# Kernel optimization log

Hardware: AMD Instinct MI355X
Metric: run time of the kernel (lower is better)

## Reference

```python
import jax, jax.numpy as jnp
import numpy as np

UNITS = 128

def setup_inputs() -> dict:
    key = jax.random.key(0)
    ks = jax.random.split(key, 8)
    B, Te, Td, De, Dd = 4, 512, 256, 512, 512
    enc = jax.random.normal(ks[0], (B, Te, De), dtype=jnp.float32)
    dec = jax.random.normal(ks[1], (B, Td, Dd), dtype=jnp.float32)
    # Dense params (glorot-ish scale)
    W1_w = jax.random.normal(ks[2], (De, UNITS), dtype=jnp.float32) / np.sqrt(De)
    W1_b = jnp.zeros((UNITS,), dtype=jnp.float32)
    W2_w = jax.random.normal(ks[3], (Dd, UNITS), dtype=jnp.float32) / np.sqrt(Dd)
    W2_b = jnp.zeros((UNITS,), dtype=jnp.float32)
    V_w = jax.random.normal(ks[4], (UNITS, 1), dtype=jnp.float32) / np.sqrt(UNITS)
    V_b = jnp.zeros((1,), dtype=jnp.float32)
    return {"encoder_out": enc, "decoder_out": dec,
            "W1_w": W1_w, "W1_b": W1_b, "W2_w": W2_w, "W2_b": W2_b,
            "V_w": V_w, "V_b": V_b}

def reference(encoder_out, decoder_out, W1_w, W1_b, W2_w, W2_b, V_w, V_b):
    # Project once per side (faithful: Dense is applied to broadcasted tensors,
    # but Dense commutes with broadcasting so projecting first is identical math).
    enc_p = jnp.einsum('bed,du->beu', encoder_out, W1_w) + W1_b   # [B,Te,U]
    dec_p = jnp.einsum('btd,du->btu', decoder_out, W2_w) + W2_b   # [B,Td,U]
    # Broadcast add -> tanh -> V score: [B,Td,Te]
    h = jnp.tanh(enc_p[:, None, :, :] + dec_p[:, :, None, :])     # [B,Td,Te,U]
    score = jnp.einsum('bteu,u->bte', h, V_w[:, 0]) + V_b[0]      # [B,Td,Te]
    attn_weights = jax.nn.softmax(score, axis=-1)
    context = jnp.einsum('bte,bed->btd', attn_weights, encoder_out)  # [B,Td,De]
    return (context, attn_weights)
```

## Files before the change

kernel.cpp:

```cpp
#include <hip/hip_runtime.h>

#define B  4
#define TE 512
#define TD 256
#define DE 512
#define U  128

__device__ __forceinline__ float fast_tanh(float x){
    float e = __builtin_amdgcn_exp2f(x * 2.8853900817779268f);
    return 1.0f - 2.0f * __builtin_amdgcn_rcpf(e + 1.0f);
}

__global__ __launch_bounds__(256) void proj_fused_kernel(
        const float* __restrict__ enc, const float* __restrict__ dec,
        const float* __restrict__ W1w, const float* __restrict__ W1b,
        const float* __restrict__ W2w, const float* __restrict__ W2b,
        float* __restrict__ encT, float* __restrict__ decp){
    __shared__ float4 Xs[8 * 128];
    float* T = (float*)Xs;
    const int tid = threadIdx.x;

    const bool is_enc = blockIdx.x < 256;
    const float *X, *W, *bias; int r0;
    if (is_enc){ r0 = blockIdx.x * 8;         X = enc; W = W1w; bias = W1b; }
    else       { r0 = (blockIdx.x - 256) * 8; X = dec; W = W2w; bias = W2b; }

    const float4* Xg = (const float4*)(X + (size_t)r0 * 512);
    #pragma unroll
    for (int j = 0; j < 4; ++j)
        Xs[j * 256 + tid] = Xg[j * 256 + tid];
    __syncthreads();

    const int q = tid & 31;
    const int g = tid >> 5;
    const float4* W4 = (const float4*)W;

    float4 acc = ((const float4*)bias)[q];

    #pragma unroll 2
    for (int d0 = 0; d0 < 512; d0 += 4){
        float4 xr = Xs[g * 128 + (d0 >> 2)];
        float4 w0 = W4[(d0 + 0) * 32 + q];
        float4 w1 = W4[(d0 + 1) * 32 + q];
        float4 w2 = W4[(d0 + 2) * 32 + q];
        float4 w3 = W4[(d0 + 3) * 32 + q];
        acc.x += xr.x*w0.x + xr.y*w1.x + xr.z*w2.x + xr.w*w3.x;
        acc.y += xr.x*w0.y + xr.y*w1.y + xr.z*w2.y + xr.w*w3.y;
        acc.z += xr.x*w0.z + xr.y*w1.z + xr.z*w2.z + xr.w*w3.z;
        acc.w += xr.x*w0.w + xr.y*w1.w + xr.z*w2.w + xr.w*w3.w;
    }

    if (is_enc){
        __syncthreads();
        T[(4*q + 0)*9 + g] = acc.x;
        T[(4*q + 1)*9 + g] = acc.y;
        T[(4*q + 2)*9 + g] = acc.z;
        T[(4*q + 3)*9 + g] = acc.w;
        __syncthreads();
        if (tid < 128){
            const int u  = tid;
            const int b  = r0 >> 9;
            const int et = r0 & 511;
            float4 lo = make_float4(T[u*9+0], T[u*9+1], T[u*9+2], T[u*9+3]);
            float4 hi = make_float4(T[u*9+4], T[u*9+5], T[u*9+6], T[u*9+7]);
            float4* row = (float4*)encT + (size_t)(b*U + u)*128 + (et >> 2);
            row[0] = lo; row[1] = hi;
        }
    } else {
        ((float4*)decp)[(size_t)(r0 + g) * 32 + q] = acc;
    }
}

__global__ __launch_bounds__(256) void score_kernel(
        const float* __restrict__ encT, const float* __restrict__ decp,
        const float* __restrict__ Vw, float* __restrict__ attn_out){
    __shared__ float4 dp4[64];
    __shared__ float4 vv4[32];
    __shared__ float redm[4], reds[4];
    const float* dpf = (const float*)dp4;
    const float* vvf = (const float*)vv4;
    const int tid = threadIdx.x;
    const int b  = blockIdx.x >> 7;
    const int t0 = (blockIdx.x & 127) * 2;

    if (tid < 64)       dp4[tid] = ((const float4*)decp)[(size_t)(b*TD + t0 + (tid>>5))*32 + (tid&31)];
    else if (tid < 96)  vv4[tid - 64] = ((const float4*)Vw)[tid - 64];
    __syncthreads();

    const int t  = tid >> 7;
    const int eq = tid & 127;
    const float4* E = (const float4*)encT + (size_t)b*U*128 + eq;

    float4 s = make_float4(0.f, 0.f, 0.f, 0.f);
    #pragma unroll 4
    for (int u = 0; u < U; ++u){
        float4 A = E[(size_t)u * 128];
        float d = dpf[t*128 + u];
        float v = vvf[u];
        s.x += fast_tanh(A.x + d) * v;
        s.y += fast_tanh(A.y + d) * v;
        s.z += fast_tanh(A.z + d) * v;
        s.w += fast_tanh(A.w + d) * v;
    }

    float m = fmaxf(fmaxf(s.x, s.y), fmaxf(s.z, s.w));
    for (int o = 32; o > 0; o >>= 1) m = fmaxf(m, __shfl_xor(m, o));
    const int w = tid >> 6;
    if ((tid & 63) == 0) redm[w] = m;
    __syncthreads();
    m = fmaxf(redm[2*t], redm[2*t + 1]);

    const float L2E = 1.4426950408889634f;
    float4 p;
    p.x = __builtin_amdgcn_exp2f((s.x - m) * L2E);
    p.y = __builtin_amdgcn_exp2f((s.y - m) * L2E);
    p.z = __builtin_amdgcn_exp2f((s.z - m) * L2E);
    p.w = __builtin_amdgcn_exp2f((s.w - m) * L2E);
    float sl = (p.x + p.y) + (p.z + p.w);
    for (int o = 32; o > 0; o >>= 1) sl += __shfl_xor(sl, o);
    if ((tid & 63) == 0) reds[w] = sl;
    __syncthreads();
    float inv = __builtin_amdgcn_rcpf(reds[2*t] + reds[2*t + 1]);

    p.x *= inv; p.y *= inv; p.z *= inv; p.w *= inv;
    ((float4*)attn_out)[(size_t)(b*TD + t0 + t)*128 + eq] = p;
}

__global__ __launch_bounds__(512) void context_kernel(
        const float* __restrict__ enc, const float* __restrict__ attn,
        float* __restrict__ ctx_out){
    __shared__ float4 at4[8 * 128];
    __shared__ float4 red4[8 * 256];
    const int tid = threadIdx.x;
    const int dh = blockIdx.x & 1;
    const int b  = (blockIdx.x >> 1) & 3;
    const int t0 = (blockIdx.x >> 3) * 8;
    const int dq = tid & 63;
    const int eq = tid >> 6;

    const float4* A4 = (const float4*)(attn + (size_t)(b*TD + t0) * TE);
    at4[tid]       = A4[tid];
    at4[tid + 512] = A4[tid + 512];
    __syncthreads();

    float4 acc[8];
    #pragma unroll
    for (int t = 0; t < 8; ++t) acc[t] = make_float4(0.f, 0.f, 0.f, 0.f);

    const float4* eb = (const float4*)enc + (size_t)(b*TE)*128 + dh*64 + dq;
    for (int ec = 0; ec < 16; ++ec){
        const int e0 = eq*64 + ec*4;
        float4 x0 = eb[(size_t)(e0 + 0) * 128];
        float4 x1 = eb[(size_t)(e0 + 1) * 128];
        float4 x2 = eb[(size_t)(e0 + 2) * 128];
        float4 x3 = eb[(size_t)(e0 + 3) * 128];
        #pragma unroll
        for (int t = 0; t < 8; ++t){
            float4 w = at4[t*128 + (e0 >> 2)];
            acc[t].x += x0.x*w.x + x1.x*w.y + x2.x*w.z + x3.x*w.w;
            acc[t].y += x0.y*w.x + x1.y*w.y + x2.y*w.z + x3.y*w.w;
            acc[t].z += x0.z*w.x + x1.z*w.y + x2.z*w.z + x3.z*w.w;
            acc[t].w += x0.w*w.x + x1.w*w.y + x2.w*w.z + x3.w*w.w;
        }
    }

    for (int step = 4; step >= 1; step >>= 1){
        if (eq >= step && eq < 2*step){
            #pragma unroll
            for (int t = 0; t < 8; ++t)
                red4[t*256 + (eq - step)*64 + dq] = acc[t];
        }
        __syncthreads();
        if (eq < step){
            #pragma unroll
            for (int t = 0; t < 8; ++t){
                float4 r = red4[t*256 + eq*64 + dq];
                acc[t].x += r.x; acc[t].y += r.y; acc[t].z += r.z; acc[t].w += r.w;
            }
        }
        __syncthreads();
    }

    if (eq == 0){
        float4* ob = (float4*)ctx_out + (size_t)(b*TD + t0)*128 + dh*64 + dq;
        #pragma unroll
        for (int t = 0; t < 8; ++t) ob[t*128] = acc[t];
    }
}

extern "C" void kernel_launch(void* const* d_in, const int* in_sizes, int n_in,
                              void* d_out, int out_size, void* d_ws, size_t ws_size,
                              hipStream_t stream){
    const float* enc = (const float*)d_in[0];
    const float* dec = (const float*)d_in[1];
    const float* W1w = (const float*)d_in[2];
    const float* W1b = (const float*)d_in[3];
    const float* W2w = (const float*)d_in[4];
    const float* W2b = (const float*)d_in[5];
    const float* Vw  = (const float*)d_in[6];

    float* encT = (float*)d_ws;
    float* decp = encT + (size_t)B*U*TE;

    float* outp     = (float*)d_out;
    float* attn_out = outp + (size_t)B*TD*DE;

    hipLaunchKernelGGL(proj_fused_kernel, dim3(384), dim3(256), 0, stream,
                       enc, dec, W1w, W1b, W2w, W2b, encT, decp);
    hipLaunchKernelGGL(score_kernel, dim3(B*TD/2), dim3(256), 0, stream,
                       encT, decp, Vw, attn_out);
    hipLaunchKernelGGL(context_kernel, dim3(B*TD/8*2), dim3(512), 0, stream,
                       enc, attn_out, outp);
}
```

Before: 134.4 us.

## Factor tanh as exp products precomputed in projection; process four decoder rows per block

```diff
diff --git a/kernel.cpp b/kernel.cpp
--- a/kernel.cpp
+++ b/kernel.cpp
@@ -6,12 +6,7 @@
 #define DE 512
 #define U  128
 
-__device__ __forceinline__ float fast_tanh(float x){
-    float e = __builtin_amdgcn_exp2f(x * 2.8853900817779268f);
-    return 1.0f - 2.0f * __builtin_amdgcn_rcpf(e + 1.0f);
-}
-
-__global__ __launch_bounds__(256) void proj_fused_kernel(
+__global__ __launch_bounds__(128) void proj_fused_kernel(
         const float* __restrict__ enc, const float* __restrict__ dec,
         const float* __restrict__ W1w, const float* __restrict__ W1b,
         const float* __restrict__ W2w, const float* __restrict__ W2b,
@@ -27,103 +22,151 @@
 
     const float4* Xg = (const float4*)(X + (size_t)r0 * 512);
     #pragma unroll
-    for (int j = 0; j < 4; ++j)
-        Xs[j * 256 + tid] = Xg[j * 256 + tid];
+    for (int j = 0; j < 8; ++j)
+        Xs[j * 128 + tid] = Xg[j * 128 + tid];
     __syncthreads();
 
     const int q = tid & 31;
     const int g = tid >> 5;
     const float4* W4 = (const float4*)W;
 
-    float4 acc = ((const float4*)bias)[q];
+    float4 acc0 = ((const float4*)bias)[q];
+    float4 acc1 = acc0;
 
     #pragma unroll 2
     for (int d0 = 0; d0 < 512; d0 += 4){
-        float4 xr = Xs[g * 128 + (d0 >> 2)];
+        float4 x0 = Xs[g * 128 + (d0 >> 2)];
+        float4 x1 = Xs[(g + 4) * 128 + (d0 >> 2)];
         float4 w0 = W4[(d0 + 0) * 32 + q];
         float4 w1 = W4[(d0 + 1) * 32 + q];
         float4 w2 = W4[(d0 + 2) * 32 + q];
         float4 w3 = W4[(d0 + 3) * 32 + q];
-        acc.x += xr.x*w0.x + xr.y*w1.x + xr.z*w2.x + xr.w*w3.x;
-        acc.y += xr.x*w0.y + xr.y*w1.y + xr.z*w2.y + xr.w*w3.y;
-        acc.z += xr.x*w0.z + xr.y*w1.z + xr.z*w2.z + xr.w*w3.z;
-        acc.w += xr.x*w0.w + xr.y*w1.w + xr.z*w2.w + xr.w*w3.w;
-    }
+        acc0.x += x0.x*w0.x + x0.y*w1.x + x0.z*w2.x + x0.w*w3.x;
+        acc0.y += x0.x*w0.y + x0.y*w1.y + x0.z*w2.y + x0.w*w3.y;
+        acc0.z += x0.x*w0.z + x0.y*w1.z + x0.z*w2.z + x0.w*w3.z;
+        acc0.w += x0.x*w0.w + x0.y*w1.w + x0.z*w2.w + x0.w*w3.w;
+        acc1.x += x1.x*w0.x + x1.y*w1.x + x1.z*w2.x + x1.w*w3.x;
+        acc1.y += x1.x*w0.y + x1.y*w1.y + x1.z*w2.y + x1.w*w3.y;
+        acc1.z += x1.x*w0.z + x1.y*w1.z + x1.z*w2.z + x1.w*w3.z;
+        acc1.w += x1.x*w0.w + x1.y*w1.w + x1.z*w2.w + x1.w*w3.w;
+    }
+
+    const float C2 = 2.8853900817779268f;
+    acc0.x = __builtin_amdgcn_exp2f(acc0.x * C2);
+    acc0.y = __builtin_amdgcn_exp2f(acc0.y * C2);
+    acc0.z = __builtin_amdgcn_exp2f(acc0.z * C2);
+    acc0.w = __builtin_amdgcn_exp2f(acc0.w * C2);
+    acc1.x = __builtin_amdgcn_exp2f(acc1.x * C2);
+    acc1.y = __builtin_amdgcn_exp2f(acc1.y * C2);
+    acc1.z = __builtin_amdgcn_exp2f(acc1.z * C2);
+    acc1.w = __builtin_amdgcn_exp2f(acc1.w * C2);
 
     if (is_enc){
         __syncthreads();
-        T[(4*q + 0)*9 + g] = acc.x;
-        T[(4*q + 1)*9 + g] = acc.y;
-        T[(4*q + 2)*9 + g] = acc.z;
-        T[(4*q + 3)*9 + g] = acc.w;
-        __syncthreads();
-        if (tid < 128){
-            const int u  = tid;
-            const int b  = r0 >> 9;
-            const int et = r0 & 511;
-            float4 lo = make_float4(T[u*9+0], T[u*9+1], T[u*9+2], T[u*9+3]);
-            float4 hi = make_float4(T[u*9+4], T[u*9+5], T[u*9+6], T[u*9+7]);
-            float4* row = (float4*)encT + (size_t)(b*U + u)*128 + (et >> 2);
-            row[0] = lo; row[1] = hi;
-        }
+        T[(4*q + 0)*9 + g]     = acc0.x;
+        T[(4*q + 1)*9 + g]     = acc0.y;
+        T[(4*q + 2)*9 + g]     = acc0.z;
+        T[(4*q + 3)*9 + g]     = acc0.w;
+        T[(4*q + 0)*9 + g + 4] = acc1.x;
+        T[(4*q + 1)*9 + g + 4] = acc1.y;
+        T[(4*q + 2)*9 + g + 4] = acc1.z;
+        T[(4*q + 3)*9 + g + 4] = acc1.w;
+        __syncthreads();
+        const int u  = tid;
+        const int b  = r0 >> 9;
+        const int et = r0 & 511;
+        float4 lo = make_float4(T[u*9+0], T[u*9+1], T[u*9+2], T[u*9+3]);
+        float4 hi = make_float4(T[u*9+4], T[u*9+5], T[u*9+6], T[u*9+7]);
+        float4* row = (float4*)encT + (size_t)(b*U + u)*128 + (et >> 2);
+        row[0] = lo; row[1] = hi;
     } else {
-        ((float4*)decp)[(size_t)(r0 + g) * 32 + q] = acc;
+        ((float4*)decp)[(size_t)(r0 + g)     * 32 + q] = acc0;
+        ((float4*)decp)[(size_t)(r0 + g + 4) * 32 + q] = acc1;
     }
 }
 
 __global__ __launch_bounds__(256) void score_kernel(
         const float* __restrict__ encT, const float* __restrict__ decp,
         const float* __restrict__ Vw, float* __restrict__ attn_out){
-    __shared__ float4 dp4[64];
+    __shared__ float4 dp4[128];
     __shared__ float4 vv4[32];
-    __shared__ float redm[4], reds[4];
+    __shared__ float redma[4], redmb[4], redsa[4], redsb[4];
     const float* dpf = (const float*)dp4;
     const float* vvf = (const float*)vv4;
     const int tid = threadIdx.x;
-    const int b  = blockIdx.x >> 7;
-    const int t0 = (blockIdx.x & 127) * 2;
-
-    if (tid < 64)       dp4[tid] = ((const float4*)decp)[(size_t)(b*TD + t0 + (tid>>5))*32 + (tid&31)];
-    else if (tid < 96)  vv4[tid - 64] = ((const float4*)Vw)[tid - 64];
-    __syncthreads();
-
-    const int t  = tid >> 7;
+    const int b  = blockIdx.x >> 6;
+    const int t0 = (blockIdx.x & 63) * 4;
+
+    if (tid < 128){
+        dp4[tid] = ((const float4*)decp)[(size_t)(b*TD + t0 + (tid>>5))*32 + (tid&31)];
+    } else if (tid < 160){
+        float4 v = ((const float4*)Vw)[tid - 128];
+        vv4[tid - 128] = make_float4(-2.f*v.x, -2.f*v.y, -2.f*v.z, -2.f*v.w);
+    }
+    __syncthreads();
+
+    const int th = tid >> 7;
     const int eq = tid & 127;
     const float4* E = (const float4*)encT + (size_t)b*U*128 + eq;
-
-    float4 s = make_float4(0.f, 0.f, 0.f, 0.f);
+    const float* dA = dpf + th * 128;
+    const float* dB = dpf + (2 + th) * 128;
+
+    float4 sa = make_float4(0.f, 0.f, 0.f, 0.f);
+    float4 sb = make_float4(0.f, 0.f, 0.f, 0.f);
     #pragma unroll 4
     for (int u = 0; u < U; ++u){
         float4 A = E[(size_t)u * 128];
-        float d = dpf[t*128 + u];
-        float v = vvf[u];
-        s.x += fast_tanh(A.x + d) * v;
-        s.y += fast_tanh(A.y + d) * v;
-        s.z += fast_tanh(A.z + d) * v;
-        s.w += fast_tanh(A.w + d) * v;
-    }
-
-    float m = fmaxf(fmaxf(s.x, s.y), fmaxf(s.z, s.w));
-    for (int o = 32; o > 0; o >>= 1) m = fmaxf(m, __shfl_xor(m, o));
+        float da = dA[u];
+        float db = dB[u];
+        float wv = vvf[u];
+        sa.x += wv * __builtin_amdgcn_rcpf(fmaf(A.x, da, 1.0f));
+        sa.y += wv * __builtin_amdgcn_rcpf(fmaf(A.y, da, 1.0f));
+        sa.z += wv * __builtin_amdgcn_rcpf(fmaf(A.z, da, 1.0f));
+        sa.w += wv * __builtin_amdgcn_rcpf(fmaf(A.w, da, 1.0f));
+        sb.x += wv * __builtin_amdgcn_rcpf(fmaf(A.x, db, 1.0f));
+        sb.y += wv * __builtin_amdgcn_rcpf(fmaf(A.y, db, 1.0f));
+        sb.z += wv * __builtin_amdgcn_rcpf(fmaf(A.z, db, 1.0f));
+        sb.w += wv * __builtin_amdgcn_rcpf(fmaf(A.w, db, 1.0f));
+    }
+
+    float ma = fmaxf(fmaxf(sa.x, sa.y), fmaxf(sa.z, sa.w));
+    float mb = fmaxf(fmaxf(sb.x, sb.y), fmaxf(sb.z, sb.w));
+    for (int o = 32; o > 0; o >>= 1){
+        ma = fmaxf(ma, __shfl_xor(ma, o));
+        mb = fmaxf(mb, __shfl_xor(mb, o));
+    }
     const int w = tid >> 6;
-    if ((tid & 63) == 0) redm[w] = m;
-    __syncthreads();
-    m = fmaxf(redm[2*t], redm[2*t + 1]);
+    if ((tid & 63) == 0){ redma[w] = ma; redmb[w] = mb; }
+    __syncthreads();
+    ma = fmaxf(redma[2*th], redma[2*th + 1]);
+    mb = fmaxf(redmb[2*th], redmb[2*th + 1]);
 
     const float L2E = 1.4426950408889634f;
-    float4 p;
-    p.x = __builtin_amdgcn_exp2f((s.x - m) * L2E);
-    p.y = __builtin_amdgcn_exp2f((s.y - m) * L2E);
-    p.z = __builtin_amdgcn_exp2f((s.z - m) * L2E);
-    p.w = __builtin_amdgcn_exp2f((s.w - m) * L2E);
-    float sl = (p.x + p.y) + (p.z + p.w);
-    for (int o = 32; o > 0; o >>= 1) sl += __shfl_xor(sl, o);
-    if ((tid & 63) == 0) reds[w] = sl;
-    __syncthreads();
-    float inv = __builtin_amdgcn_rcpf(reds[2*t] + reds[2*t + 1]);
-
-    p.x *= inv; p.y *= inv; p.z *= inv; p.w *= inv;
-    ((float4*)attn_out)[(size_t)(b*TD + t0 + t)*128 + eq] = p;
+    float4 pa, pb;
+    pa.x = __builtin_amdgcn_exp2f((sa.x - ma) * L2E);
+    pa.y = __builtin_amdgcn_exp2f((sa.y - ma) * L2E);
+    pa.z = __builtin_amdgcn_exp2f((sa.z - ma) * L2E);
+    pa.w = __builtin_amdgcn_exp2f((sa.w - ma) * L2E);
+    pb.x = __builtin_amdgcn_exp2f((sb.x - mb) * L2E);
+    pb.y = __builtin_amdgcn_exp2f((sb.y - mb) * L2E);
+    pb.z = __builtin_amdgcn_exp2f((sb.z - mb) * L2E);
+    pb.w = __builtin_amdgcn_exp2f((sb.w - mb) * L2E);
+    float sla = (pa.x + pa.y) + (pa.z + pa.w);
+    float slb = (pb.x + pb.y) + (pb.z + pb.w);
+    for (int o = 32; o > 0; o >>= 1){
+        sla += __shfl_xor(sla, o);
+        slb += __shfl_xor(slb, o);
+    }
+    if ((tid & 63) == 0){ redsa[w] = sla; redsb[w] = slb; }
+    __syncthreads();
+    float inva = __builtin_amdgcn_rcpf(redsa[2*th] + redsa[2*th + 1]);
+    float invb = __builtin_amdgcn_rcpf(redsb[2*th] + redsb[2*th + 1]);
+
+    float4* O = (float4*)attn_out;
+    O[(size_t)(b*TD + t0 + th)*128 + eq] =
+        make_float4(pa.x*inva, pa.y*inva, pa.z*inva, pa.w*inva);
+    O[(size_t)(b*TD + t0 + 2 + th)*128 + eq] =
+        make_float4(pb.x*invb, pb.y*invb, pb.z*invb, pb.w*invb);
 }
 
 __global__ __launch_bounds__(512) void context_kernel(
@@ -205,9 +248,9 @@
     float* outp     = (float*)d_out;
     float* attn_out = outp + (size_t)B*TD*DE;
 
-    hipLaunchKernelGGL(proj_fused_kernel, dim3(384), dim3(256), 0, stream,
+    hipLaunchKernelGGL(proj_fused_kernel, dim3(384), dim3(128), 0, stream,
                        enc, dec, W1w, W1b, W2w, W2b, encT, decp);
-    hipLaunchKernelGGL(score_kernel, dim3(B*TD/2), dim3(256), 0, stream,
+    hipLaunchKernelGGL(score_kernel, dim3(B*TD/4), dim3(256), 0, stream,
                        encT, decp, Vw, attn_out);
     hipLaunchKernelGGL(context_kernel, dim3(B*TD/8*2), dim3(512), 0, stream,
                        enc, attn_out, outp);
```

Result: faster. 121.1 us (-9.9%).

## Factor tanh via precomputed exponentials and split reductions across thread groups

Applied to the files above, without the earlier changes.

```diff
diff --git a/kernel.cpp b/kernel.cpp
--- a/kernel.cpp
+++ b/kernel.cpp
@@ -6,10 +6,16 @@
 #define DE 512
 #define U  128
 
-__device__ __forceinline__ float fast_tanh(float x){
-    float e = __builtin_amdgcn_exp2f(x * 2.8853900817779268f);
-    return 1.0f - 2.0f * __builtin_amdgcn_rcpf(e + 1.0f);
-}
+#define RCPF(x)  __builtin_amdgcn_rcpf(x)
+#define EXP2F(x) __builtin_amdgcn_exp2f(x)
+
+#define ROWFMA(ar, xr) \
+    ar.x += xr.x*w0.x + xr.y*w1.x + xr.z*w2.x + xr.w*w3.x; \
+    ar.y += xr.x*w0.y + xr.y*w1.y + xr.z*w2.y + xr.w*w3.y; \
+    ar.z += xr.x*w0.z + xr.y*w1.z + xr.z*w2.z + xr.w*w3.z; \
+    ar.w += xr.x*w0.w + xr.y*w1.w + xr.z*w2.w + xr.w*w3.w;
+
+#define ADD4(d, s) d.x += s.x; d.y += s.y; d.z += s.z; d.w += s.w;
 
 __global__ __launch_bounds__(256) void proj_fused_kernel(
         const float* __restrict__ enc, const float* __restrict__ dec,
@@ -17,6 +23,7 @@
         const float* __restrict__ W2w, const float* __restrict__ W2b,
         float* __restrict__ encT, float* __restrict__ decp){
     __shared__ float4 Xs[8 * 128];
+    __shared__ float4 Ps[3 * 4 * 64];
     float* T = (float*)Xs;
     const int tid = threadIdx.x;
 
@@ -31,99 +38,215 @@
         Xs[j * 256 + tid] = Xg[j * 256 + tid];
     __syncthreads();
 
-    const int q = tid & 31;
-    const int g = tid >> 5;
+    const int q  = tid & 31;
+    const int g  = (tid >> 5) & 1;
+    const int ds = tid >> 6;
     const float4* W4 = (const float4*)W;
 
-    float4 acc = ((const float4*)bias)[q];
-
+    float4 a0, a1, a2, a3;
+    a0 = a1 = a2 = a3 = make_float4(0.f, 0.f, 0.f, 0.f);
+
+    const int dbase = ds * 128;
     #pragma unroll 2
-    for (int d0 = 0; d0 < 512; d0 += 4){
-        float4 xr = Xs[g * 128 + (d0 >> 2)];
+    for (int dd = 0; dd < 128; dd += 4){
+        const int d0 = dbase + dd;
+        const int xq = d0 >> 2;
+        float4 x0 = Xs[(g + 0) * 128 + xq];
+        float4 x1 = Xs[(g + 2) * 128 + xq];
+        float4 x2 = Xs[(g + 4) * 128 + xq];
+        float4 x3 = Xs[(g + 6) * 128 + xq];
         float4 w0 = W4[(d0 + 0) * 32 + q];
         float4 w1 = W4[(d0 + 1) * 32 + q];
         float4 w2 = W4[(d0 + 2) * 32 + q];
         float4 w3 = W4[(d0 + 3) * 32 + q];
-        acc.x += xr.x*w0.x + xr.y*w1.x + xr.z*w2.x + xr.w*w3.x;
-        acc.y += xr.x*w0.y + xr.y*w1.y + xr.z*w2.y + xr.w*w3.y;
-        acc.z += xr.x*w0.z + xr.y*w1.z + xr.z*w2.z + xr.w*w3.z;
-        acc.w += xr.x*w0.w + xr.y*w1.w + xr.z*w2.w + xr.w*w3.w;
-    }
-
-    if (is_enc){
-        __syncthreads();
-        T[(4*q + 0)*9 + g] = acc.x;
-        T[(4*q + 1)*9 + g] = acc.y;
-        T[(4*q + 2)*9 + g] = acc.z;
-        T[(4*q + 3)*9 + g] = acc.w;
-        __syncthreads();
-        if (tid < 128){
-            const int u  = tid;
-            const int b  = r0 >> 9;
-            const int et = r0 & 511;
-            float4 lo = make_float4(T[u*9+0], T[u*9+1], T[u*9+2], T[u*9+3]);
-            float4 hi = make_float4(T[u*9+4], T[u*9+5], T[u*9+6], T[u*9+7]);
-            float4* row = (float4*)encT + (size_t)(b*U + u)*128 + (et >> 2);
-            row[0] = lo; row[1] = hi;
-        }
-    } else {
-        ((float4*)decp)[(size_t)(r0 + g) * 32 + q] = acc;
+        ROWFMA(a0, x0)
+        ROWFMA(a1, x1)
+        ROWFMA(a2, x2)
+        ROWFMA(a3, x3)
+    }
+
+    const int slot = (g << 5) | q;
+    if (ds){
+        Ps[((ds-1)*4 + 0)*64 + slot] = a0;
+        Ps[((ds-1)*4 + 1)*64 + slot] = a1;
+        Ps[((ds-1)*4 + 2)*64 + slot] = a2;
+        Ps[((ds-1)*4 + 3)*64 + slot] = a3;
+    }
+    __syncthreads();
+
+    if (ds == 0){
+        #pragma unroll
+        for (int p = 0; p < 3; ++p){
+            float4 r;
+            r = Ps[(p*4 + 0)*64 + slot]; ADD4(a0, r)
+            r = Ps[(p*4 + 1)*64 + slot]; ADD4(a1, r)
+            r = Ps[(p*4 + 2)*64 + slot]; ADD4(a2, r)
+            r = Ps[(p*4 + 3)*64 + slot]; ADD4(a3, r)
+        }
+        float4 bq = ((const float4*)bias)[q];
+        ADD4(a0, bq) ADD4(a1, bq) ADD4(a2, bq) ADD4(a3, bq)
+
+        const float C2 = 2.8853900817779268f;
+        a0.x = EXP2F(a0.x*C2); a0.y = EXP2F(a0.y*C2); a0.z = EXP2F(a0.z*C2); a0.w = EXP2F(a0.w*C2);
+        a1.x = EXP2F(a1.x*C2); a1.y = EXP2F(a1.y*C2); a1.z = EXP2F(a1.z*C2); a1.w = EXP2F(a1.w*C2);
+        a2.x = EXP2F(a2.x*C2); a2.y = EXP2F(a2.y*C2); a2.z = EXP2F(a2.z*C2); a2.w = EXP2F(a2.w*C2);
+        a3.x = EXP2F(a3.x*C2); a3.y = EXP2F(a3.y*C2); a3.z = EXP2F(a3.z*C2); a3.w = EXP2F(a3.w*C2);
+
+        if (is_enc){
+            T[(4*q+0)*9 + g + 0] = a0.x; T[(4*q+1)*9 + g + 0] = a0.y;
+            T[(4*q+2)*9 + g + 0] = a0.z; T[(4*q+3)*9 + g + 0] = a0.w;
+            T[(4*q+0)*9 + g + 2] = a1.x; T[(4*q+1)*9 + g + 2] = a1.y;
+            T[(4*q+2)*9 + g + 2] = a1.z; T[(4*q+3)*9 + g + 2] = a1.w;
+            T[(4*q+0)*9 + g + 4] = a2.x; T[(4*q+1)*9 + g + 4] = a2.y;
+            T[(4*q+2)*9 + g + 4] = a2.z; T[(4*q+3)*9 + g + 4] = a2.w;
+            T[(4*q+0)*9 + g + 6] = a3.x; T[(4*q+1)*9 + g + 6] = a3.y;
+            T[(4*q+2)*9 + g + 6] = a3.z; T[(4*q+3)*9 + g + 6] = a3.w;
+        } else {
+            float4* D = (float4*)decp;
+            D[(size_t)(r0 + g + 0) * 32 + q] = a0;
+            D[(size_t)(r0 + g + 2) * 32 + q] = a1;
+            D[(size_t)(r0 + g + 4) * 32 + q] = a2;
+            D[(size_t)(r0 + g + 6) * 32 + q] = a3;
+        }
+    }
+    __syncthreads();
+
+    if (is_enc && tid < 128){
+        const int u  = tid;
+        const int bb = r0 >> 9;
+        const int et = r0 & 511;
+        float4 lo = make_float4(T[u*9+0], T[u*9+1], T[u*9+2], T[u*9+3]);
+        float4 hi = make_float4(T[u*9+4], T[u*9+5], T[u*9+6], T[u*9+7]);
+        float4* row = (float4*)encT + (size_t)(bb*U + u)*128 + (et >> 2);
+        row[0] = lo; row[1] = hi;
     }
 }
 
-__global__ __launch_bounds__(256) void score_kernel(
+#define TANH_ACC(s, dv) \
+    s.x += wv * RCPF(fmaf(A.x, dv, 1.0f)); \
+    s.y += wv * RCPF(fmaf(A.y, dv, 1.0f)); \
+    s.z += wv * RCPF(fmaf(A.z, dv, 1.0f)); \
+    s.w += wv * RCPF(fmaf(A.w, dv, 1.0f));
+
+__global__ __launch_bounds__(512) void score_kernel(
         const float* __restrict__ encT, const float* __restrict__ decp,
         const float* __restrict__ Vw, float* __restrict__ attn_out){
-    __shared__ float4 dp4[64];
+    __shared__ float4 dp4[128];
     __shared__ float4 vv4[32];
-    __shared__ float redm[4], reds[4];
+    __shared__ float4 Pp[3 * 4 * 128];
+    __shared__ float redm[8], reds[8];
     const float* dpf = (const float*)dp4;
     const float* vvf = (const float*)vv4;
     const int tid = threadIdx.x;
-    const int b  = blockIdx.x >> 7;
-    const int t0 = (blockIdx.x & 127) * 2;
-
-    if (tid < 64)       dp4[tid] = ((const float4*)decp)[(size_t)(b*TD + t0 + (tid>>5))*32 + (tid&31)];
-    else if (tid < 96)  vv4[tid - 64] = ((const float4*)Vw)[tid - 64];
-    __syncthreads();
-
-    const int t  = tid >> 7;
+    const int b  = blockIdx.x >> 6;
+    const int t0 = (blockIdx.x & 63) * 4;
+
+    if (tid < 128){
+        dp4[tid] = ((const float4*)decp)[(size_t)(b*TD + t0 + (tid>>5))*32 + (tid&31)];
+    } else if (tid < 160){
+        float4 v = ((const float4*)Vw)[tid - 128];
+        vv4[tid - 128] = make_float4(-2.f*v.x, -2.f*v.y, -2.f*v.z, -2.f*v.w);
+    }
+    __syncthreads();
+
+    const int uh = tid >> 7;
     const int eq = tid & 127;
-    const float4* E = (const float4*)encT + (size_t)b*U*128 + eq;
-
-    float4 s = make_float4(0.f, 0.f, 0.f, 0.f);
+    const int u0 = uh * 32;
+
+    const float4* E  = (const float4*)encT + (size_t)b*U*128 + (size_t)u0*128 + eq;
+    const float* dt0 = dpf + 0*128 + u0;
+    const float* dt1 = dpf + 1*128 + u0;
+    const float* dt2 = dpf + 2*128 + u0;
+    const float* dt3 = dpf + 3*128 + u0;
+    const float* vv  = vvf + u0;
+
+    float4 s0, s1, s2, s3;
+    s0 = s1 = s2 = s3 = make_float4(0.f, 0.f, 0.f, 0.f);
+
     #pragma unroll 4
-    for (int u = 0; u < U; ++u){
+    for (int u = 0; u < 32; ++u){
         float4 A = E[(size_t)u * 128];
-        float d = dpf[t*128 + u];
-        float v = vvf[u];
-        s.x += fast_tanh(A.x + d) * v;
-        s.y += fast_tanh(A.y + d) * v;
-        s.z += fast_tanh(A.z + d) * v;
-        s.w += fast_tanh(A.w + d) * v;
-    }
-
-    float m = fmaxf(fmaxf(s.x, s.y), fmaxf(s.z, s.w));
-    for (int o = 32; o > 0; o >>= 1) m = fmaxf(m, __shfl_xor(m, o));
+        float d0 = dt0[u], d1 = dt1[u], d2 = dt2[u], d3 = dt3[u];
+        float wv = vv[u];
+        TANH_ACC(s0, d0)
+        TANH_ACC(s1, d1)
+        TANH_ACC(s2, d2)
+        TANH_ACC(s3, d3)
+    }
+
+    if (uh){
+        Pp[((uh-1)*4 + 0)*128 + eq] = s0;
+        Pp[((uh-1)*4 + 1)*128 + eq] = s1;
+        Pp[((uh-1)*4 + 2)*128 + eq] = s2;
+        Pp[((uh-1)*4 + 3)*128 + eq] = s3;
+    }
+    __syncthreads();
+
+    float4 p0, p1, p2, p3;
+    float m0, m1, m2, m3;
     const int w = tid >> 6;
-    if ((tid & 63) == 0) redm[w] = m;
-    __syncthreads();
-    m = fmaxf(redm[2*t], redm[2*t + 1]);
-
-    const float L2E = 1.4426950408889634f;
-    float4 p;
-    p.x = __builtin_amdgcn_exp2f((s.x - m) * L2E);
-    p.y = __builtin_amdgcn_exp2f((s.y - m) * L2E);
-    p.z = __builtin_amdgcn_exp2f((s.z - m) * L2E);
-    p.w = __builtin_amdgcn_exp2f((s.w - m) * L2E);
-    float sl = (p.x + p.y) + (p.z + p.w);
-    for (int o = 32; o > 0; o >>= 1) sl += __shfl_xor(sl, o);
-    if ((tid & 63) == 0) reds[w] = sl;
-    __syncthreads();
-    float inv = __builtin_amdgcn_rcpf(reds[2*t] + reds[2*t + 1]);
-
-    p.x *= inv; p.y *= inv; p.z *= inv; p.w *= inv;
-    ((float4*)attn_out)[(size_t)(b*TD + t0 + t)*128 + eq] = p;
+    if (uh == 0){
+        #pragma unroll
+        for (int p = 0; p < 3; ++p){
+            float4 r;
+            r = Pp[(p*4 + 0)*128 + eq]; ADD4(s0, r)
+            r = Pp[(p*4 + 1)*128 + eq]; ADD4(s1, r)
+            r = Pp[(p*4 + 2)*128 + eq]; ADD4(s2, r)
+            r = Pp[(p*4 + 3)*128 + eq]; ADD4(s3, r)
+        }
+        m0 = fmaxf(fmaxf(s0.x, s0.y), fmaxf(s0.z, s0.w));
+        m1 = fmaxf(fmaxf(s1.x, s1.y), fmaxf(s1.z, s1.w));
+        m2 = fmaxf(fmaxf(s2.x, s2.y), fmaxf(s2.z, s2.w));
+        m3 = fmaxf(fmaxf(s3.x, s3.y), fmaxf(s3.z, s3.w));
+        for (int o = 32; o > 0; o >>= 1){
+            m0 = fmaxf(m0, __shfl_xor(m0, o));
+            m1 = fmaxf(m1, __shfl_xor(m1, o));
+            m2 = fmaxf(m2, __shfl_xor(m2, o));
+            m3 = fmaxf(m3, __shfl_xor(m3, o));
+        }
+        if ((tid & 63) == 0){
+            redm[0*2 + w] = m0; redm[1*2 + w] = m1;
+            redm[2*2 + w] = m2; redm[3*2 + w] = m3;
+        }
+    }
+    __syncthreads();
+    if (uh == 0){
+        m0 = fmaxf(redm[0], redm[1]); m1 = fmaxf(redm[2], redm[3]);
+        m2 = fmaxf(redm[4], redm[5]); m3 = fmaxf(redm[6], redm[7]);
+        const float L2E = 1.4426950408889634f;
+        p0.x = EXP2F((s0.x-m0)*L2E); p0.y = EXP2F((s0.y-m0)*L2E);
+        p0.z = EXP2F((s0.z-m0)*L2E); p0.w = EXP2F((s0.w-m0)*L2E);
+        p1.x = EXP2F((s1.x-m1)*L2E); p1.y = EXP2F((s1.y-m1)*L2E);
+        p1.z = EXP2F((s1.z-m1)*L2E); p1.w = EXP2F((s1.w-m1)*L2E);
+        p2.x = EXP2F((s2.x-m2)*L2E); p2.y = EXP2F((s2.y-m2)*L2E);
+        p2.z = EXP2F((s2.z-m2)*L2E); p2.w = EXP2F((s2.w-m2)*L2E);
+        p3.x = EXP2F((s3.x-m3)*L2E); p3.y = EXP2F((s3.y-m3)*L2E);
+        p3.z = EXP2F((s3.z-m3)*L2E); p3.w = EXP2F((s3.w-m3)*L2E);
+        float l0 = (p0.x+p0.y)+(p0.z+p0.w);
+        float l1 = (p1.x+p1.y)+(p1.z+p1.w);
+        float l2 = (p2.x+p2.y)+(p2.z+p2.w);
+        float l3 = (p3.x+p3.y)+(p3.z+p3.w);
+        for (int o = 32; o > 0; o >>= 1){
+            l0 += __shfl_xor(l0, o); l1 += __shfl_xor(l1, o);
+            l2 += __shfl_xor(l2, o); l3 += __shfl_xor(l3, o);
+        }
+        if ((tid & 63) == 0){
+            reds[0*2 + w] = l0; reds[1*2 + w] = l1;
+            reds[2*2 + w] = l2; reds[3*2 + w] = l3;
+        }
+    }
+    __syncthreads();
+    if (uh == 0){
+        float i0 = RCPF(reds[0] + reds[1]);
+        float i1 = RCPF(reds[2] + reds[3]);
+        float i2 = RCPF(reds[4] + reds[5]);
+        float i3 = RCPF(reds[6] + reds[7]);
+        float4* O = (float4*)attn_out;
+        O[(size_t)(b*TD + t0 + 0)*128 + eq] = make_float4(p0.x*i0, p0.y*i0, p0.z*i0, p0.w*i0);
+        O[(size_t)(b*TD + t0 + 1)*128 + eq] = make_float4(p1.x*i1, p1.y*i1, p1.z*i1, p1.w*i1);
+        O[(size_t)(b*TD + t0 + 2)*128 + eq] = make_float4(p2.x*i2, p2.y*i2, p2.z*i2, p2.w*i2);
+        O[(size_t)(b*TD + t0 + 3)*128 + eq] = make_float4(p3.x*i3, p3.y*i3, p3.z*i3, p3.w*i3);
+    }
 }
 
 __global__ __launch_bounds__(512) void context_kernel(
@@ -207,7 +330,7 @@
 
     hipLaunchKernelGGL(proj_fused_kernel, dim3(384), dim3(256), 0, stream,
                        enc, dec, W1w, W1b, W2w, W2b, encT, decp);
-    hipLaunchKernelGGL(score_kernel, dim3(B*TD/2), dim3(256), 0, stream,
+    hipLaunchKernelGGL(score_kernel, dim3(B*TD/4), dim3(512), 0, stream,
                        encT, decp, Vw, attn_out);
     hipLaunchKernelGGL(context_kernel, dim3(B*TD/8*2), dim3(512), 0, stream,
                        enc, attn_out, outp);
```

Result: faster. 113.4 us (-15.7%).
